# Optimization experiments

Measured on AMD Instinct MI355X. Metric: run time of the kernel, lower is better.

Reference implementation:

```python
import jax, jax.numpy as jnp
import numpy as np

B, O, C, HID, H, W = 4, 8, 256, 128, 64, 64
STEPS = 2  # message passing steps


def _conv3x3(x, w, b):
    # x: [N,Cin,H,W], w: [Cout,Cin,3,3]
    y = jax.lax.conv_general_dilated(x, w, window_strides=(1, 1), padding='SAME',
                                     dimension_numbers=('NCHW', 'OIHW', 'NCHW'))
    return y + b[None, :, None, None]


def setup_inputs() -> dict:
    key = jax.random.key(0)
    ks = jax.random.split(key, 6)
    return {
        'batch_node_feats': jax.random.normal(ks[0], (B, C, H, W), jnp.float32),
        'batch_previous_masks': jax.random.uniform(ks[1], (B, O, H, W), jnp.float32),
        'batch_valid_indices': jnp.ones((B, O), jnp.bool_),
        'batch_previous_states': jnp.zeros((B, O), jnp.float32),  # unused (use_temporal_features=False)
        'enc_w': jax.random.normal(ks[2], (HID, C + 1, 3, 3), jnp.float32) * 0.02,
        'enc_b': jnp.zeros((HID,), jnp.float32),
        'gcn_w': jax.random.normal(ks[3], (HID, 2 * HID, 3, 3), jnp.float32) * 0.02,
        'gcn_b': jnp.zeros((HID,), jnp.float32),
        'ro_w': jax.random.normal(ks[4], (1, C + HID, 3, 3), jnp.float32) * 0.02,
        'ro_b': jnp.zeros((1,), jnp.float32),
    }


def reference(batch_node_feats, batch_previous_masks, batch_valid_indices,
              batch_previous_states, enc_w, enc_b, gcn_w, gcn_b, ro_w, ro_b):
    # All objects valid (batch_valid_indices all True) -> fully vectorized over B and O.
    feats = jnp.broadcast_to(batch_node_feats[:, None], (B, O, C, H, W))
    # Mask encoder: per-object state from frame feats + previous object mask.
    enc_in = jnp.concatenate([feats, batch_previous_masks[:, :, None]], axis=2)
    states = jax.nn.relu(_conv3x3(enc_in.reshape(B * O, C + 1, H, W), enc_w, enc_b))
    states = states.reshape(B, O, HID, H, W)
    # Fully-connected message passing: neighbors of i = all objects except i.
    for _ in range(STEPS):
        agg = states.sum(axis=1, keepdims=True) - states  # sum over others
        gcn_in = jnp.concatenate([states, agg], axis=2).reshape(B * O, 2 * HID, H, W)
        states = jax.nn.relu(_conv3x3(gcn_in, gcn_w, gcn_b)).reshape(B, O, HID, H, W)
    # Readout: per-object mask logits -> sigmoid.
    ro_in = jnp.concatenate([feats, states], axis=2).reshape(B * O, C + HID, H, W)
    out_masks = jax.nn.sigmoid(_conv3x3(ro_in, ro_w, ro_b)).reshape(B, O, H, W)
    return out_masks  # out_states is None when use_temporal_features=False
```

## Files before the change

### kernel.cpp

```cpp
#include <hip/hip_runtime.h>
#include <math.h>


typedef unsigned short ushort_t;
typedef _Float16 f16x8 __attribute__((ext_vector_type(8)));
typedef _Float16 f16x2 __attribute__((ext_vector_type(2)));
typedef float f32x4 __attribute__((ext_vector_type(4)));

#define GLDS(gsrc, ldst)                                                      \
    __builtin_amdgcn_global_load_lds(                                         \
        (const __attribute__((address_space(1))) unsigned int*)(gsrc),        \
        (__attribute__((address_space(3))) unsigned int*)(ldst), 16, 0, 0)

#define WAITVM0() asm volatile("s_waitcnt vmcnt(0)" ::: "memory")
#define WAITVM2() asm volatile("s_waitcnt vmcnt(2)" ::: "memory")
#define WAITVM6() asm volatile("s_waitcnt vmcnt(6)" ::: "memory")
#define WAITLGKM0() asm volatile("s_waitcnt lgkmcnt(0)" ::: "memory")

__device__ __forceinline__ ushort_t f2h(float f) {
    _Float16 h = (_Float16)f;
    return *(ushort_t*)&h;
}
__device__ __forceinline__ float h2f(ushort_t u) {
    _Float16 h = *(_Float16*)&u;
    return (float)h;
}

__global__ __launch_bounds__(256) void prep_all(
    const float* __restrict__ feats, const float* __restrict__ enc_w,
    const float* __restrict__ gcn_w, const float* __restrict__ ro_w,
    ushort_t* __restrict__ featsT, ushort_t* __restrict__ WencF,
    ushort_t* __restrict__ WgcnS, ushort_t* __restrict__ WgcnD,
    ushort_t* __restrict__ WroQ, ushort_t* __restrict__ WroS)
{
    __shared__ float tile[64][65];
    int bid = blockIdx.x, t = threadIdx.x;
    if (bid < 1024) {
        int pt = bid & 63, ct = (bid >> 6) & 3, img = bid >> 8;
        int px_l = t & 63;
        const float* src = feats + ((size_t)img * 256 + ct * 64) * 4096 + pt * 64;
#pragma unroll
        for (int j = 0; j < 16; ++j) {
            int ci_l = (t >> 6) + j * 4;
            tile[px_l][ci_l] = src[(size_t)ci_l * 4096 + px_l];
        }
        __syncthreads();
        int px = t >> 2;
#pragma unroll
        for (int j = 0; j < 2; ++j) {
            int c8 = ((t & 3) + j * 4) * 8;
            uint4 v; ushort_t* pv = (ushort_t*)&v;
#pragma unroll
            for (int k = 0; k < 8; ++k) pv[k] = f2h(tile[px][c8 + k]);
            int cc = ct * 2 + (c8 >> 5);
            *(uint4*)(featsT + ((size_t)img * 8 + cc) * 131072 +
                      (size_t)(pt * 64 + px) * 32 + (c8 & 31)) = v;
        }
        return;
    }
    int i = (bid - 1024) * 256 + t;
    if (i < 294912) {
        int ci32 = i & 31, co = (i >> 5) & 127, tc = i >> 12;
        int tt = tc >> 3, cc = tc & 7, ci = cc * 32 + ci32;
        WencF[i] = f2h(enc_w[(co * 257 + ci) * 9 + tt]);
    } else if (i < 442368) {
        int j = i - 294912;
        int ci32 = j & 31, co = (j >> 5) & 127, tc = j >> 12;
        int tt = tc >> 2, cc = tc & 3, ci = cc * 32 + ci32;
        WgcnS[j] = f2h(gcn_w[(co * 256 + 128 + ci) * 9 + tt]);
    } else if (i < 589824) {
        int j = i - 442368;
        int ci32 = j & 31, co = (j >> 5) & 127, tc = j >> 12;
        int tt = tc >> 2, cc = tc & 3, ci = cc * 32 + ci32;
        WgcnD[j] = f2h(gcn_w[(co * 256 + ci) * 9 + tt] -
                       gcn_w[(co * 256 + 128 + ci) * 9 + tt]);
    } else if (i < 592128) {
        int j = i - 589824;
        int k = j & 7, r = j >> 3;
        int tt = r % 9, cq = r / 9, q = cq & 3, cc = cq >> 2;
        WroQ[j] = f2h(ro_w[(cc * 32 + q * 8 + k) * 9 + tt]);
    } else if (i < 593280) {
        int j = i - 592128;
        int k = j & 7, r = j >> 3;
        int tt = r % 9, cq = r / 9, q = cq & 3, cc = cq >> 2;
        WroS[j] = f2h(ro_w[(256 + cc * 32 + q * 8 + k) * 9 + tt]);
    }
}

template<int NCCBLK, bool FUSE, bool SUMIN>
__global__ __launch_bounds__(256, 3) void conv_k(
    const ushort_t* __restrict__ x, const ushort_t* __restrict__ W,
    ushort_t* __restrict__ out,
    const ushort_t* __restrict__ addp, const float* __restrict__ bias,
    int ncc_img)
{
    __shared__ ushort_t raw[25088];
    ushort_t* xs = raw;
    ushort_t* wlds = raw + 16896;
    ushort_t* eb16 = raw;

    const int rp = blockIdx.x, img = blockIdx.y, kz = blockIdx.z;
    const int row0 = rp * 2;
    const int cc0 = kz * NCCBLK;
    const int nchunk = 9 * NCCBLK;
    const int tid = threadIdx.x;
    const int w = tid >> 6, lane = tid & 63, lq = lane >> 4, lr = lane & 15;
    const int cg = w >> 1, pg = w & 1;

    const size_t objstride = (size_t)ncc_img * 131072;
    const ushort_t* xb = SUMIN ? x + (size_t)img * 8 * objstride
                               : x + (size_t)img * objstride;
    const int aoff0 = (cg * 64 + lr) * 32 + (lq ^ ((lr >> 1) & 3)) * 8;

    if (tid < 64) {
        int b = tid >> 5, r = (tid >> 3) & 3, c = (tid >> 2) & 1, s = tid & 3;
        *(uint4*)(xs + b * 8448 + r * 2112 + (c ? 65 : 0) * 32 + s * 8) =
            make_uint4(0, 0, 0, 0);
    }

    f32x4 acc[4][4];
#pragma unroll
    for (int a = 0; a < 4; ++a)
#pragma unroll
        for (int p = 0; p < 4; ++p) acc[a][p] = (f32x4){0.f, 0.f, 0.f, 0.f};

    const int gy = row0 - 1 + w;
    const bool row_ok = (unsigned)gy < 64u;
#define STAGE_ACT(cc_, buf_)                                                    \
    {                                                                           \
        ushort_t* dstrow = xs + (buf_) * 8448 + w * 2112;                       \
        if (row_ok) {                                                           \
            const ushort_t* src = xb + (size_t)(cc_) * 131072 + (size_t)gy * 2048; \
            if constexpr (SUMIN) {                                              \
                _Pragma("unroll")                                               \
                for (int u_ = 0; u_ < 4; ++u_) {                                \
                    f16x8 a_ = {0, 0, 0, 0, 0, 0, 0, 0};                        \
                    _Pragma("unroll")                                           \
                    for (int o_ = 0; o_ < 8; ++o_)                              \
                        a_ = a_ + *(const f16x8*)(src + (size_t)o_ * objstride + \
                                                  u_ * 512 + lane * 8);         \
                    int colp_ = 1 + u_ * 16 + (lane >> 2);                      \
                    int ssw_ = (lane & 3) ^ ((colp_ >> 1) & 3);                 \
                    *(f16x8*)(dstrow + colp_ * 32 + ssw_ * 8) = a_;             \
                }                                                               \
            } else {                                                            \
                _Pragma("unroll")                                               \
                for (int u_ = 0; u_ < 4; ++u_) {                                \
                    int colp_ = 1 + u_ * 16 + (lane >> 2);                      \
                    int ssw_ = (lane & 3) ^ ((colp_ >> 1) & 3);                 \
                    GLDS(src + (size_t)(colp_ - 1) * 32 + ssw_ * 8,             \
                         dstrow + 32 + u_ * 512);                               \
                }                                                               \
            }                                                                   \
        } else {                                                                \
            _Pragma("unroll")                                                   \
            for (int u_ = 0; u_ < 4; ++u_)                                      \
                *(uint4*)(dstrow + 32 + u_ * 512 + lane * 8) =                  \
                    make_uint4(0, 0, 0, 0);                                     \
        }                                                                       \
    }
#define STAGE_W(t_, cc_, buf_)                                                  \
    {                                                                           \
        const ushort_t* src = W + ((size_t)((t_) * ncc_img + (cc_)) * 4096);    \
        ushort_t* dst = wlds + (buf_) * 4096;                                   \
        _Pragma("unroll")                                                       \
        for (int j_ = 0; j_ < 2; ++j_) {                                        \
            int co_ = (w * 2 + j_) * 16 + (lane >> 2);                          \
            int ssw_ = (lane & 3) ^ ((co_ >> 1) & 3);                           \
            GLDS(src + co_ * 32 + ssw_ * 8, dst + (w * 2 + j_) * 512);          \
        }                                                                       \
    }

    STAGE_ACT(cc0, 0);
    STAGE_W(0, cc0, 0);
    STAGE_W(1, cc0, 1);
    WAITLGKM0();

#pragma unroll
    for (int ccl = 0; ccl < NCCBLK; ++ccl) {
        const int cc = cc0 + ccl;
        const int xbuf = ccl & 1;
#pragma unroll
        for (int t = 0; t < 9; ++t) {
            const int kc = ccl * 9 + t;
            if (kc == nchunk - 1) { WAITVM0(); }
            else if ((t == 5 || t == 6) && (ccl + 1 < NCCBLK)) { WAITVM6(); }
            else { WAITVM2(); }
            __builtin_amdgcn_s_barrier();

            const int dy = t / 3, dx = t - 3 * dy;
            const ushort_t* wl = wlds + (kc & 1) * 4096 + aoff0;
            const int colb = dx + lr;
            const int swb = lq ^ ((colb >> 1) & 3);
            const ushort_t* xl = xs + xbuf * 8448 + (pg + dy) * 2112 +
                                 colb * 32 + swb * 8;
            f16x8 A0 = *(const f16x8*)(wl);
            f16x8 A1 = *(const f16x8*)(wl + 512);
            f16x8 A2 = *(const f16x8*)(wl + 1024);
            f16x8 A3 = *(const f16x8*)(wl + 1536);
            f16x8 B0 = *(const f16x8*)(xl);
            f16x8 B1 = *(const f16x8*)(xl + 512);
            f16x8 B2 = *(const f16x8*)(xl + 1024);
            f16x8 B3 = *(const f16x8*)(xl + 1536);

            if (kc + 2 < nchunk) {
                WAITLGKM0();
                __builtin_amdgcn_sched_barrier(0);
                __builtin_amdgcn_s_barrier();
                STAGE_W((kc + 2) % 9, cc0 + (kc + 2) / 9, kc & 1);
                if (t == 4 && ccl + 1 < NCCBLK) STAGE_ACT(cc + 1, xbuf ^ 1);
            }

            __builtin_amdgcn_s_setprio(1);
            acc[0][0] = __builtin_amdgcn_mfma_f32_16x16x32_f16(A0, B0, acc[0][0], 0, 0, 0);
            acc[1][0] = __builtin_amdgcn_mfma_f32_16x16x32_f16(A1, B0, acc[1][0], 0, 0, 0);
            acc[2][0] = __builtin_amdgcn_mfma_f32_16x16x32_f16(A2, B0, acc[2][0], 0, 0, 0);
            acc[3][0] = __builtin_amdgcn_mfma_f32_16x16x32_f16(A3, B0, acc[3][0], 0, 0, 0);
            acc[0][1] = __builtin_amdgcn_mfma_f32_16x16x32_f16(A0, B1, acc[0][1], 0, 0, 0);
            acc[1][1] = __builtin_amdgcn_mfma_f32_16x16x32_f16(A1, B1, acc[1][1], 0, 0, 0);
            acc[2][1] = __builtin_amdgcn_mfma_f32_16x16x32_f16(A2, B1, acc[2][1], 0, 0, 0);
            acc[3][1] = __builtin_amdgcn_mfma_f32_16x16x32_f16(A3, B1, acc[3][1], 0, 0, 0);
            acc[0][2] = __builtin_amdgcn_mfma_f32_16x16x32_f16(A0, B2, acc[0][2], 0, 0, 0);
            acc[1][2] = __builtin_amdgcn_mfma_f32_16x16x32_f16(A1, B2, acc[1][2], 0, 0, 0);
            acc[2][2] = __builtin_amdgcn_mfma_f32_16x16x32_f16(A2, B2, acc[2][2], 0, 0, 0);
            acc[3][2] = __builtin_amdgcn_mfma_f32_16x16x32_f16(A3, B2, acc[3][2], 0, 0, 0);
            acc[0][3] = __builtin_amdgcn_mfma_f32_16x16x32_f16(A0, B3, acc[0][3], 0, 0, 0);
            acc[1][3] = __builtin_amdgcn_mfma_f32_16x16x32_f16(A1, B3, acc[1][3], 0, 0, 0);
            acc[2][3] = __builtin_amdgcn_mfma_f32_16x16x32_f16(A2, B3, acc[2][3], 0, 0, 0);
            acc[3][3] = __builtin_amdgcn_mfma_f32_16x16x32_f16(A3, B3, acc[3][3], 0, 0, 0);
            __builtin_amdgcn_s_setprio(0);
        }
    }

    ushort_t* obase = out + (size_t)(kz * gridDim.y + img) * 524288;
    const int b4 = img >> 3;
#pragma unroll
    for (int r = 0; r < 2; ++r) {
        __syncthreads();
        if (pg == r) {
#pragma unroll
            for (int cf = 0; cf < 4; ++cf)
#pragma unroll
                for (int pf = 0; pf < 4; ++pf) {
                    int px = pf * 16 + lr;
                    int co_l = cg * 64 + cf * 16 + lq * 4;
                    ushort_t pk[4];
#pragma unroll
                    for (int j = 0; j < 4; ++j) pk[j] = f2h(acc[cf][pf][j]);
                    *(uint2*)(eb16 + px * 136 + co_l) = *(uint2*)pk;
                }
        }
        __syncthreads();
#pragma unroll
        for (int k2 = 0; k2 < 4; ++k2) {
            int i = tid + k2 * 256;
            int px = i >> 4, c16 = i & 15;
            int pxg = (row0 + r) * 64 + px;
            size_t coff = (size_t)(c16 >> 2) * 131072 + (size_t)pxg * 32 + (c16 & 3) * 8;
            uint4 v = *(uint4*)(eb16 + px * 136 + c16 * 8);
            if constexpr (FUSE) {
                const ushort_t* vp = (const ushort_t*)&v;
                float vv[8];
#pragma unroll
                for (int k = 0; k < 8; ++k) vv[k] = h2f(vp[k]) + bias[c16 * 8 + k];
#pragma unroll
                for (int p = 0; p < 4; ++p) {
                    uint4 av = *(const uint4*)(addp + (size_t)(p * 4 + b4) * 524288 + coff);
                    const ushort_t* ap = (const ushort_t*)&av;
#pragma unroll
                    for (int k = 0; k < 8; ++k) vv[k] += h2f(ap[k]);
                }
                uint4 sv; ushort_t* sp = (ushort_t*)&sv;
#pragma unroll
                for (int k = 0; k < 8; ++k) sp[k] = f2h(fmaxf(vv[k], 0.f));
                *(uint4*)(obase + coff) = sv;
            } else {
                *(uint4*)(obase + coff) = v;
            }
        }
    }
#undef STAGE_ACT
#undef STAGE_W
}

__global__ __launch_bounds__(256) void enc_obj_ro(
    const float* __restrict__ masks, const float* __restrict__ enc_w,
    const float* __restrict__ enc_b, const ushort_t* __restrict__ U1p,
    const ushort_t* __restrict__ featsT, const ushort_t* __restrict__ WroQ,
    ushort_t* __restrict__ S, ushort_t* __restrict__ USum,
    float* __restrict__ YR)
{
    int bid = blockIdx.x, tid = threadIdx.x;
    if (bid >= 1024) {
        int i = (bid - 1024) * 256 + tid;
        int cu = i & 31, px = (i >> 5) & 4095, b = i >> 17;
        int cc = cu >> 2, q = cu & 3;
        int y = px >> 6, xcol = px & 63;
        const ushort_t* wp = WroQ + (size_t)(cc * 4 + q) * 72;
        float wreg[9][8];
#pragma unroll
        for (int t = 0; t < 9; ++t) {
            uint4 wv = *(const uint4*)(wp + t * 8);
            const ushort_t* wq = (const ushort_t*)&wv;
#pragma unroll
            for (int k = 0; k < 8; ++k) wreg[t][k] = h2f(wq[k]);
        }
        const ushort_t* fb = featsT + (size_t)(b * 8 + cc) * 131072 + q * 8;
        float acc = 0.f;
#pragma unroll
        for (int dy = 0; dy < 3; ++dy) {
            int gy = y + dy - 1;
            if ((unsigned)gy >= 64u) continue;
#pragma unroll
            for (int dx = 0; dx < 3; ++dx) {
                int gx = xcol + dx - 1;
                if ((unsigned)gx >= 64u) continue;
                uint4 v = *(const uint4*)(fb + (size_t)(gy * 64 + gx) * 32);
                const ushort_t* vp = (const ushort_t*)&v;
#pragma unroll
                for (int k = 0; k < 8; ++k)
                    acc = fmaf(h2f(vp[k]), wreg[dy * 3 + dx][k], acc);
            }
        }
#pragma unroll
        for (int d = 16; d >= 1; d >>= 1) acc += __shfl_down(acc, d, 32);
        if (cu == 0) YR[b * 4096 + px] = acc;
        return;
    }
    int i = bid * 256 + tid;
    int s = i & 3, px = (i >> 2) & 4095, cc = (i >> 14) & 3, b = i >> 16;
    int co = cc * 32 + s * 8;
    int y = px >> 6, xx = px & 63;
    size_t coff = (size_t)cc * 131072 + (size_t)px * 32 + s * 8;
    float base[8];
#pragma unroll
    for (int k = 0; k < 8; ++k) base[k] = enc_b[co + k];
#pragma unroll
    for (int p = 0; p < 4; ++p) {
        uint4 v = *(const uint4*)(U1p + (size_t)(p * 4 + b) * 524288 + coff);
        const ushort_t* vp = (const ushort_t*)&v;
#pragma unroll
        for (int k = 0; k < 8; ++k) base[k] += h2f(vp[k]);
    }
    float wm[8][9];
#pragma unroll
    for (int k = 0; k < 8; ++k) {
        const float* wp = enc_w + (size_t)((co + k) * 257 + 256) * 9;
#pragma unroll
        for (int t = 0; t < 9; ++t) wm[k][t] = wp[t];
    }
    float sacc[8] = {0, 0, 0, 0, 0, 0, 0, 0};
#pragma unroll
    for (int o = 0; o < 8; ++o) {
        const float* m = masks + (size_t)(b * 8 + o) * 4096;
        float mt[9];
#pragma unroll
        for (int dy = 0; dy < 3; ++dy)
#pragma unroll
            for (int dx = 0; dx < 3; ++dx) {
                int gy_ = y + dy - 1, gx = xx + dx - 1;
                mt[dy * 3 + dx] =
                    ((unsigned)gy_ < 64u && (unsigned)gx < 64u) ? m[gy_ * 64 + gx] : 0.f;
            }
        uint4 sv; ushort_t* sp = (ushort_t*)&sv;
#pragma unroll
        for (int k = 0; k < 8; ++k) {
            float acc = base[k];
#pragma unroll
            for (int t = 0; t < 9; ++t) acc = fmaf(mt[t], wm[k][t], acc);
            acc = fmaxf(acc, 0.f);
            sacc[k] += acc;
            sp[k] = f2h(acc);
        }
        *(uint4*)(S + (size_t)(b * 8 + o) * 524288 + coff) = sv;
    }
    uint4 sv; ushort_t* sp = (ushort_t*)&sv;
#pragma unroll
    for (int k = 0; k < 8; ++k) sp[k] = f2h(sacc[k]);
    *(uint4*)(USum + (size_t)b * 524288 + coff) = sv;
}

__global__ __launch_bounds__(256) void ro_obj(
    const ushort_t* __restrict__ S, const ushort_t* __restrict__ WroS,
    const float* __restrict__ ro_b, const float* __restrict__ YR,
    float* __restrict__ out)
{
    __shared__ ushort_t sl[12288 + 1152];
    ushort_t* wl = sl + 12288;
    const int rq = blockIdx.x;
    const int n  = blockIdx.y;
    const int b  = n >> 3;
    const int tid = threadIdx.x;
    const int lane = tid & 63;
    const int yl = tid >> 6, x = tid & 63;

    if (tid < 144)
        *(uint4*)(wl + tid * 8) = *(const uint4*)(WroS + tid * 8);

    float acc = 0.f;
#pragma unroll
    for (int cc = 0; cc < 4; ++cc) {
        __syncthreads();
        const ushort_t* sb = S + ((size_t)n * 4 + cc) * 131072;
#pragma unroll
        for (int k = 0; k < 6; ++k) {
            int c = (tid >> 6) * 6 + k;
            int j = c >> 2, qd = c & 3;
            int gyr = rq * 4 - 1 + j;
            ushort_t* dst = sl + j * 2048 + qd * 512;
            if ((unsigned)gyr < 64u) {
                int colq = qd * 16 + (lane >> 2);
                GLDS(sb + (size_t)gyr * 2048 + colq * 32 +
                         ((lane & 3) ^ ((colq >> 1) & 3)) * 8,
                     dst);
            } else {
                *(uint4*)(dst + lane * 8) = make_uint4(0, 0, 0, 0);
            }
        }
        __syncthreads();
#pragma unroll
        for (int dy = 0; dy < 3; ++dy) {
            const ushort_t* rowp = sl + (yl + dy) * 2048;
#pragma unroll
            for (int dx = 0; dx < 3; ++dx) {
                int gx = x + dx - 1;
                if ((unsigned)gx >= 64u) continue;
                const int tap = dy * 3 + dx;
#pragma unroll
                for (int q = 0; q < 4; ++q) {
                    f16x8 sv = *(const f16x8*)(rowp + gx * 32 +
                                               (q ^ ((gx >> 1) & 3)) * 8);
                    f16x8 wv = *(const f16x8*)(wl + ((cc * 4 + q) * 9 + tap) * 8);
                    f16x2 s0 = {sv[0], sv[1]}, s1 = {sv[2], sv[3]};
                    f16x2 s2 = {sv[4], sv[5]}, s3 = {sv[6], sv[7]};
                    f16x2 w0 = {wv[0], wv[1]}, w1 = {wv[2], wv[3]};
                    f16x2 w2 = {wv[4], wv[5]}, w3 = {wv[6], wv[7]};
                    acc = __builtin_amdgcn_fdot2(s0, w0, acc, false);
                    acc = __builtin_amdgcn_fdot2(s1, w1, acc, false);
                    acc = __builtin_amdgcn_fdot2(s2, w2, acc, false);
                    acc = __builtin_amdgcn_fdot2(s3, w3, acc, false);
                }
            }
        }
    }
    int pxg = (rq * 4 + yl) * 64 + x;
    float v = acc + YR[b * 4096 + pxg] + ro_b[0];
    out[(size_t)n * 4096 + pxg] = 1.f / (1.f + __expf(-v));
}

extern "C" void kernel_launch(void* const* d_in, const int* in_sizes, int n_in,
                              void* d_out, int out_size, void* d_ws, size_t ws_size,
                              hipStream_t stream)
{
    const float* feats = (const float*)d_in[0];
    const float* masks = (const float*)d_in[1];
    const float* enc_w = (const float*)d_in[4];
    const float* enc_b = (const float*)d_in[5];
    const float* gcn_w = (const float*)d_in[6];
    const float* gcn_b = (const float*)d_in[7];
    const float* ro_w  = (const float*)d_in[8];
    const float* ro_b  = (const float*)d_in[9];
    float* out = (float*)d_out;

    ushort_t* WencF  = (ushort_t*)d_ws;
    ushort_t* WgcnS  = WencF + 294912;
    ushort_t* WgcnD  = WgcnS + 147456;
    ushort_t* WroQ   = WgcnD + 147456;
    ushort_t* WroS   = WroQ + 2304;
    ushort_t* featsT = WroS + 1152;
    ushort_t* Sa     = featsT + 4194304;
    ushort_t* Sb     = Sa + 16777216;
    ushort_t* USum   = Sb + 16777216;
    ushort_t* U1p16  = USum + 2097152;
    ushort_t* U2p16  = U1p16 + 8388608;
    float*    YR     = (float*)(U2p16 + 8388608);

    dim3 blk(256);

    prep_all<<<3344, blk, 0, stream>>>(feats, enc_w, gcn_w, ro_w,
                                       featsT, WencF, WgcnS, WgcnD, WroQ, WroS);

    conv_k<2, false, false><<<dim3(32, 4, 4), blk, 0, stream>>>(
        featsT, WencF, U1p16, nullptr, nullptr, 8);
    enc_obj_ro<<<3072, blk, 0, stream>>>(masks, enc_w, enc_b, U1p16,
                                         featsT, WroQ, Sa, USum, YR);

    conv_k<1, false, false><<<dim3(32, 4, 4), blk, 0, stream>>>(
        USum, WgcnS, U2p16, nullptr, nullptr, 4);
    conv_k<4, true, false><<<dim3(32, 32, 1), blk, 0, stream>>>(
        Sa, WgcnD, Sb, U2p16, gcn_b, 4);

    conv_k<1, false, true><<<dim3(32, 4, 4), blk, 0, stream>>>(
        Sb, WgcnS, U2p16, nullptr, nullptr, 4);
    conv_k<4, true, false><<<dim3(32, 32, 1), blk, 0, stream>>>(
        Sb, WgcnD, Sa, U2p16, gcn_b, 4);

    ro_obj<<<dim3(16, 32), blk, 0, stream>>>(Sa, WroS, ro_b, YR, out);
}
```

Before: 257.4 us.

## Add dedicated per-object GCN conv kernel with 4-row tiles and staged weights

Result: slower. 540.0 us (+109.8%).

```diff
diff --git a/kernel.cpp b/kernel.cpp
--- a/kernel.cpp
+++ b/kernel.cpp
@@ -283,6 +283,162 @@
 #undef STAGE_W
 }
 
+__global__ __launch_bounds__(256, 3) void conv_obj(
+    const ushort_t* __restrict__ x, const ushort_t* __restrict__ W,
+    ushort_t* __restrict__ out, const ushort_t* __restrict__ addp,
+    const float* __restrict__ bias)
+{
+    __shared__ ushort_t raw[24576];
+    ushort_t* xs = raw;
+    ushort_t* wlds = raw + 12288;
+    ushort_t* eb16 = raw;
+
+    const int rq = blockIdx.x, img = blockIdx.y;
+    const int row0 = rq * 4;
+    const int tid = threadIdx.x;
+    const int w = tid >> 6, lane = tid & 63, lq = lane >> 4, lr = lane & 15;
+    const int cg = w >> 1, pg = w & 1;
+
+    const ushort_t* xb = x + (size_t)img * 524288;
+    const int aoff0 = (cg * 64 + lr) * 32 + (lq ^ ((lr >> 1) & 3)) * 8;
+
+    f32x4 acc[4][8];
+#pragma unroll
+    for (int a = 0; a < 4; ++a)
+#pragma unroll
+        for (int p = 0; p < 8; ++p) acc[a][p] = (f32x4){0.f, 0.f, 0.f, 0.f};
+
+#define STAGE_ACT4(cc_)                                                         \
+    {                                                                           \
+        const ushort_t* srcb = xb + (size_t)(cc_) * 131072;                     \
+        _Pragma("unroll")                                                       \
+        for (int j_ = 0; j_ < 6; ++j_) {                                        \
+            int idx_ = w * 6 + j_, rl_ = idx_ >> 2, q_ = idx_ & 3;              \
+            int gy_ = row0 - 1 + rl_;                                           \
+            ushort_t* dst_ = xs + rl_ * 2048 + q_ * 512;                        \
+            if ((unsigned)gy_ < 64u) {                                          \
+                int col_ = q_ * 16 + (lane >> 2);                               \
+                int ss_ = (lane & 3) ^ ((col_ >> 1) & 3);                       \
+                GLDS(srcb + (size_t)gy_ * 2048 + col_ * 32 + ss_ * 8, dst_);    \
+            } else {                                                            \
+                *(uint4*)(dst_ + lane * 8) = make_uint4(0, 0, 0, 0);            \
+            }                                                                   \
+        }                                                                       \
+    }
+#define STAGE_W3(t_, cc_, buf_)                                                 \
+    {                                                                           \
+        const ushort_t* src = W + ((size_t)((t_) * 4 + (cc_)) * 4096);          \
+        ushort_t* dst = wlds + (buf_) * 4096;                                   \
+        _Pragma("unroll")                                                       \
+        for (int j_ = 0; j_ < 2; ++j_) {                                        \
+            int co_ = (w * 2 + j_) * 16 + (lane >> 2);                          \
+            int ssw_ = (lane & 3) ^ ((co_ >> 1) & 3);                           \
+            GLDS(src + co_ * 32 + ssw_ * 8, dst + (w * 2 + j_) * 512);          \
+        }                                                                       \
+    }
+
+    STAGE_ACT4(0);
+    STAGE_W3(0, 0, 0);
+    STAGE_W3(1, 0, 1);
+
+#pragma unroll
+    for (int ccl = 0; ccl < 4; ++ccl) {
+#pragma unroll
+        for (int t = 0; t < 9; ++t) {
+            const int kc = ccl * 9 + t;
+            if (t == 0) {
+                if (ccl == 0) {
+                    WAITVM2(); WAITLGKM0();
+                    __builtin_amdgcn_s_barrier();
+                } else {
+                    WAITVM2();
+                    __builtin_amdgcn_s_barrier();
+                    STAGE_ACT4(ccl);
+                    STAGE_W3((kc + 2) % 9, (kc + 2) / 9, (kc + 2) % 3);
+                    WAITVM2();
+                    WAITLGKM0();
+                    __builtin_amdgcn_s_barrier();
+                }
+            } else {
+                if (kc == 35) { WAITVM0(); } else { WAITVM2(); }
+                __builtin_amdgcn_s_barrier();
+            }
+            if ((t != 0 || ccl == 0) && kc + 2 < 36)
+                STAGE_W3((kc + 2) % 9, (kc + 2) / 9, (kc + 2) % 3);
+
+            const int dy = t / 3, dx = t - 3 * dy;
+            const ushort_t* wl = wlds + (kc % 3) * 4096 + aoff0;
+            f16x8 A0 = *(const f16x8*)(wl);
+            f16x8 A1 = *(const f16x8*)(wl + 512);
+            f16x8 A2 = *(const f16x8*)(wl + 1024);
+            f16x8 A3 = *(const f16x8*)(wl + 1536);
+
+            __builtin_amdgcn_s_setprio(1);
+#pragma unroll
+            for (int pf = 0; pf < 8; ++pf) {
+                const int rl = 2 * pg + (pf >> 2) + dy;
+                const int c = (pf & 3) * 16 + lr + dx - 1;
+                const int c2 = c < 0 ? 0 : (c > 63 ? 63 : c);
+                f16x8 Bf = *(const f16x8*)(xs + rl * 2048 + c2 * 32 +
+                                           (lq ^ ((c2 >> 1) & 3)) * 8);
+                if (c != c2) Bf = (f16x8){0, 0, 0, 0, 0, 0, 0, 0};
+                acc[0][pf] = __builtin_amdgcn_mfma_f32_16x16x32_f16(A0, Bf, acc[0][pf], 0, 0, 0);
+                acc[1][pf] = __builtin_amdgcn_mfma_f32_16x16x32_f16(A1, Bf, acc[1][pf], 0, 0, 0);
+                acc[2][pf] = __builtin_amdgcn_mfma_f32_16x16x32_f16(A2, Bf, acc[2][pf], 0, 0, 0);
+                acc[3][pf] = __builtin_amdgcn_mfma_f32_16x16x32_f16(A3, Bf, acc[3][pf], 0, 0, 0);
+            }
+            __builtin_amdgcn_s_setprio(0);
+        }
+    }
+
+    ushort_t* obase = out + (size_t)img * 524288;
+    const int b4 = img >> 3;
+#pragma unroll
+    for (int r = 0; r < 4; ++r) {
+        __syncthreads();
+        if (pg == (r >> 1)) {
+            const int pb = (r & 1) * 4;
+#pragma unroll
+            for (int cf = 0; cf < 4; ++cf)
+#pragma unroll
+                for (int pf2 = 0; pf2 < 4; ++pf2) {
+                    int px = pf2 * 16 + lr;
+                    int co_l = cg * 64 + cf * 16 + lq * 4;
+                    ushort_t pk[4];
+#pragma unroll
+                    for (int j = 0; j < 4; ++j) pk[j] = f2h(acc[cf][pb + pf2][j]);
+                    *(uint2*)(eb16 + px * 136 + co_l) = *(uint2*)pk;
+                }
+        }
+        __syncthreads();
+#pragma unroll
+        for (int k2 = 0; k2 < 4; ++k2) {
+            int i = tid + k2 * 256;
+            int px = i >> 4, c16 = i & 15;
+            int pxg = (row0 + r) * 64 + px;
+            size_t coff = (size_t)(c16 >> 2) * 131072 + (size_t)pxg * 32 + (c16 & 3) * 8;
+            uint4 v = *(uint4*)(eb16 + px * 136 + c16 * 8);
+            const ushort_t* vp = (const ushort_t*)&v;
+            float vv[8];
+#pragma unroll
+            for (int k = 0; k < 8; ++k) vv[k] = h2f(vp[k]) + bias[c16 * 8 + k];
+#pragma unroll
+            for (int p = 0; p < 4; ++p) {
+                uint4 av = *(const uint4*)(addp + (size_t)(p * 4 + b4) * 524288 + coff);
+                const ushort_t* ap = (const ushort_t*)&av;
+#pragma unroll
+                for (int k = 0; k < 8; ++k) vv[k] += h2f(ap[k]);
+            }
+            uint4 sv; ushort_t* sp = (ushort_t*)&sv;
+#pragma unroll
+            for (int k = 0; k < 8; ++k) sp[k] = f2h(fmaxf(vv[k], 0.f));
+            *(uint4*)(obase + coff) = sv;
+        }
+    }
+#undef STAGE_ACT4
+#undef STAGE_W3
+}
+
 __global__ __launch_bounds__(256) void enc_obj_ro(
     const float* __restrict__ masks, const float* __restrict__ enc_w,
     const float* __restrict__ enc_b, const ushort_t* __restrict__ U1p,
@@ -487,13 +643,11 @@
 
     conv_k<1, false, false><<<dim3(32, 4, 4), blk, 0, stream>>>(
         USum, WgcnS, U2p16, nullptr, nullptr, 4);
-    conv_k<4, true, false><<<dim3(32, 32, 1), blk, 0, stream>>>(
-        Sa, WgcnD, Sb, U2p16, gcn_b, 4);
+    conv_obj<<<dim3(16, 32), blk, 0, stream>>>(Sa, WgcnD, Sb, U2p16, gcn_b);
 
     conv_k<1, false, true><<<dim3(32, 4, 4), blk, 0, stream>>>(
         Sb, WgcnS, U2p16, nullptr, nullptr, 4);
-    conv_k<4, true, false><<<dim3(32, 32, 1), blk, 0, stream>>>(
-        Sb, WgcnD, Sa, U2p16, gcn_b, 4);
+    conv_obj<<<dim3(16, 32), blk, 0, stream>>>(Sb, WgcnD, Sa, U2p16, gcn_b);
 
     ro_obj<<<dim3(16, 32), blk, 0, stream>>>(Sa, WroS, ro_b, YR, out);
 }
```

## Single-buffer activations and triple-buffer weights to drop per-chunk second barrier

Applied to the files above, without the earlier changes.

Measured after the change: 252.8 us. Within noise of the previous version (-1.8%).

```diff
diff --git a/kernel.cpp b/kernel.cpp
--- a/kernel.cpp
+++ b/kernel.cpp
@@ -14,7 +14,6 @@
 
 #define WAITVM0() asm volatile("s_waitcnt vmcnt(0)" ::: "memory")
 #define WAITVM2() asm volatile("s_waitcnt vmcnt(2)" ::: "memory")
-#define WAITVM6() asm volatile("s_waitcnt vmcnt(6)" ::: "memory")
 #define WAITLGKM0() asm volatile("s_waitcnt lgkmcnt(0)" ::: "memory")
 
 __device__ __forceinline__ ushort_t f2h(float f) {
@@ -94,9 +93,9 @@
     const ushort_t* __restrict__ addp, const float* __restrict__ bias,
     int ncc_img)
 {
-    __shared__ ushort_t raw[25088];
+    __shared__ ushort_t raw[20736];
     ushort_t* xs = raw;
-    ushort_t* wlds = raw + 16896;
+    ushort_t* wlds = raw + 8448;
     ushort_t* eb16 = raw;
 
     const int rp = blockIdx.x, img = blockIdx.y, kz = blockIdx.z;
@@ -112,9 +111,9 @@
                                : x + (size_t)img * objstride;
     const int aoff0 = (cg * 64 + lr) * 32 + (lq ^ ((lr >> 1) & 3)) * 8;
 
-    if (tid < 64) {
-        int b = tid >> 5, r = (tid >> 3) & 3, c = (tid >> 2) & 1, s = tid & 3;
-        *(uint4*)(xs + b * 8448 + r * 2112 + (c ? 65 : 0) * 32 + s * 8) =
+    if (tid < 32) {
+        int r = tid >> 3, c = (tid >> 2) & 1, s = tid & 3;
+        *(uint4*)(xs + r * 2112 + (c ? 65 : 0) * 32 + s * 8) =
             make_uint4(0, 0, 0, 0);
     }
 
@@ -126,9 +125,9 @@
 
     const int gy = row0 - 1 + w;
     const bool row_ok = (unsigned)gy < 64u;
-#define STAGE_ACT(cc_, buf_)                                                    \
+#define STAGE_ACT(cc_)                                                          \
     {                                                                           \
-        ushort_t* dstrow = xs + (buf_) * 8448 + w * 2112;                       \
+        ushort_t* dstrow = xs + w * 2112;                                       \
         if (row_ok) {                                                           \
             const ushort_t* src = xb + (size_t)(cc_) * 131072 + (size_t)gy * 2048; \
             if constexpr (SUMIN) {                                              \
@@ -159,10 +158,10 @@
                     make_uint4(0, 0, 0, 0);                                     \
         }                                                                       \
     }
-#define STAGE_W(t_, cc_, buf_)                                                  \
+#define STAGE_W(t_, cc_, slot_)                                                 \
     {                                                                           \
         const ushort_t* src = W + ((size_t)((t_) * ncc_img + (cc_)) * 4096);    \
-        ushort_t* dst = wlds + (buf_) * 4096;                                   \
+        ushort_t* dst = wlds + (slot_) * 4096;                                  \
         _Pragma("unroll")                                                       \
         for (int j_ = 0; j_ < 2; ++j_) {                                        \
             int co_ = (w * 2 + j_) * 16 + (lane >> 2);                          \
@@ -171,7 +170,7 @@
         }                                                                       \
     }
 
-    STAGE_ACT(cc0, 0);
+    STAGE_ACT(cc0);
     STAGE_W(0, cc0, 0);
     STAGE_W(1, cc0, 1);
     WAITLGKM0();
@@ -179,21 +178,28 @@
 #pragma unroll
     for (int ccl = 0; ccl < NCCBLK; ++ccl) {
         const int cc = cc0 + ccl;
-        const int xbuf = ccl & 1;
 #pragma unroll
         for (int t = 0; t < 9; ++t) {
             const int kc = ccl * 9 + t;
-            if (kc == nchunk - 1) { WAITVM0(); }
-            else if ((t == 5 || t == 6) && (ccl + 1 < NCCBLK)) { WAITVM6(); }
-            else { WAITVM2(); }
+            if (kc == nchunk - 1) { WAITVM0(); } else { WAITVM2(); }
             __builtin_amdgcn_s_barrier();
 
+            if (t == 0 && ccl > 0) {
+                STAGE_ACT(cc);
+                if (kc + 2 < nchunk)
+                    STAGE_W((kc + 2) % 9, cc0 + (kc + 2) / 9, (kc + 2) % 3);
+                WAITVM2();
+                WAITLGKM0();
+                __builtin_amdgcn_s_barrier();
+            } else if (kc + 2 < nchunk) {
+                STAGE_W((kc + 2) % 9, cc0 + (kc + 2) / 9, (kc + 2) % 3);
+            }
+
             const int dy = t / 3, dx = t - 3 * dy;
-            const ushort_t* wl = wlds + (kc & 1) * 4096 + aoff0;
+            const ushort_t* wl = wlds + (kc % 3) * 4096 + aoff0;
             const int colb = dx + lr;
             const int swb = lq ^ ((colb >> 1) & 3);
-            const ushort_t* xl = xs + xbuf * 8448 + (pg + dy) * 2112 +
-                                 colb * 32 + swb * 8;
+            const ushort_t* xl = xs + (pg + dy) * 2112 + colb * 32 + swb * 8;
             f16x8 A0 = *(const f16x8*)(wl);
             f16x8 A1 = *(const f16x8*)(wl + 512);
             f16x8 A2 = *(const f16x8*)(wl + 1024);
@@ -202,14 +208,6 @@
             f16x8 B1 = *(const f16x8*)(xl + 512);
             f16x8 B2 = *(const f16x8*)(xl + 1024);
             f16x8 B3 = *(const f16x8*)(xl + 1536);
-
-            if (kc + 2 < nchunk) {
-                WAITLGKM0();
-                __builtin_amdgcn_sched_barrier(0);
-                __builtin_amdgcn_s_barrier();
-                STAGE_W((kc + 2) % 9, cc0 + (kc + 2) / 9, kc & 1);
-                if (t == 4 && ccl + 1 < NCCBLK) STAGE_ACT(cc + 1, xbuf ^ 1);
-            }
 
             __builtin_amdgcn_s_setprio(1);
             acc[0][0] = __builtin_amdgcn_mfma_f32_16x16x32_f16(A0, B0, acc[0][0], 0, 0, 0);
```
